# Optimization experiments

Measured on AMD Instinct MI355X. Metric: run time of the kernel, lower is better.

The kernel has to match this reference:

```python
import jax, jax.numpy as jnp
import numpy as np

EMBED_DIM = 1024
ATTEN_DIM = 64


def setup_inputs() -> dict:
    key = jax.random.key(0)
    k_x, k_q, k_k, k_v = jax.random.split(key, 4)
    B, S = 4, 4096
    scale = 1.0 / np.sqrt(EMBED_DIM)
    x = jax.random.normal(k_x, (B, S, EMBED_DIM), dtype=jnp.float32)
    # torch nn.Linear weights are [out_features, in_features]
    Wq = jax.random.normal(k_q, (ATTEN_DIM, EMBED_DIM), dtype=jnp.float32) * scale
    Wk = jax.random.normal(k_k, (ATTEN_DIM, EMBED_DIM), dtype=jnp.float32) * scale
    Wv = jax.random.normal(k_v, (ATTEN_DIM, EMBED_DIM), dtype=jnp.float32) * scale
    return {"x": x, "Wq": Wq, "Wk": Wk, "Wv": Wv}


def reference(x, Wq, Wk, Wv):
    # q, k, v: [B, S, D]
    q = jnp.einsum('bse,de->bsd', x, Wq)
    k = jnp.einsum('bse,de->bsd', x, Wk)
    v = jnp.einsum('bse,de->bsd', x, Wv)
    d = k.shape[-1]
    scores = jnp.einsum('bsd,btd->bst', q, k) / jnp.sqrt(jnp.float32(d))
    S = x.shape[1]
    causal = jnp.tril(jnp.ones((S, S), dtype=bool))
    scores = jnp.where(causal[None, :, :], scores, -jnp.inf)
    attn = jax.nn.softmax(scores, axis=-1)
    return jnp.einsum('bst,btd->bsd', attn, v)
```

## Files before the change

### kernel.cpp

```cpp
#include <hip/hip_runtime.h>
#include <hip/hip_bf16.h>
#include <stdint.h>

typedef __attribute__((ext_vector_type(8))) short  short8;
typedef __attribute__((ext_vector_type(4))) short  short4v;
typedef __attribute__((ext_vector_type(4))) float  float4v;

#define MFMA16(a, b, c) __builtin_amdgcn_mfma_f32_16x16x32_bf16((a), (b), (c), 0, 0, 0)

#define S_LEN  4096
#define NBATCH 4
#define EMB    1024
#define DD     64
#define NROWS  (NBATCH * S_LEN)
#define SCL2   0.1803368801111204f

static __device__ __forceinline__ short f2bf(float f) {
  uint32_t u = __float_as_uint(f);
  return (short)((u + 0x7FFFu + ((u >> 16) & 1u)) >> 16);
}
static __device__ __forceinline__ unsigned pk2(float a, float b) {
  union { __hip_bfloat162 h; unsigned u; } z;
  z.h = __float22bfloat162_rn(make_float2(a, b));
  return z.u;
}
static __device__ __forceinline__ short8 cvt8(float4v a, float4v b) {
  union { unsigned u[4]; short8 s; } z;
  z.u[0] = pk2(a[0], a[1]); z.u[1] = pk2(a[2], a[3]);
  z.u[2] = pk2(b[0], b[1]); z.u[3] = pk2(b[2], b[3]);
  return z.s;
}
static __device__ __forceinline__ short4v cvt4(float4v a) {
  union { unsigned u[2]; short4v s; } z;
  z.u[0] = pk2(a[0], a[1]); z.u[1] = pk2(a[2], a[3]);
  return z.s;
}

__global__ void wcvt_kernel(const float* __restrict__ Wq, const float* __restrict__ Wk,
                            const float* __restrict__ Wv, short* __restrict__ Wb2) {
  const int t   = blockIdx.x * 256 + threadIdx.x;
  const int row = t >> 7;
  const int k   = (t & 127) * 8;
  const float* src = (row < 64) ? (Wq + (size_t)row * EMB)
                   : (row < 128) ? (Wk + (size_t)(row - 64) * EMB)
                                 : (Wv + (size_t)(row - 128) * EMB);
  float4v a = *(const float4v*)(src + k);
  float4v b = *(const float4v*)(src + k + 4);
  *(short8*)(Wb2 + (((k >> 5) * 192 + row) << 5) + (k & 31)) = cvt8(a, b);
}

#define ASTR 40
#define BSTR 40

__global__ __launch_bounds__(256, 2) void qkv_kernel(
    const float* __restrict__ x, const short* __restrict__ Wb2,
    short* __restrict__ Qb, short* __restrict__ Kb, short* __restrict__ Vt) {
  __shared__ short As[2][32 * ASTR];
  __shared__ short Bs[2][192 * BSTR];

  const int tid  = threadIdx.x;
  const int w    = tid >> 6;
  const int lane = tid & 63;
  const int ln   = lane & 15;
  const int quad = lane >> 4;
  const int m0   = blockIdx.x * 32;
  const int rf   = w & 1;
  const int ch   = w >> 1;

  const int ar = tid >> 3, ac = (tid & 7) * 4;
  const float* xp = x + (size_t)(m0 + ar) * EMB + ac;

  const float4v zz = {0.f, 0.f, 0.f, 0.f};
  float4v acc[6];
#pragma unroll
  for (int f = 0; f < 6; ++f) acc[f] = zz;

  float4v apf = *(const float4v*)(xp);
  short8 bpf[3];
#pragma unroll
  for (int j = 0; j < 3; ++j)
    bpf[j] = *(const short8*)(Wb2 + (j * 256 + tid) * 8);

  int buf = 0;
  for (int s = 0; s < 32; ++s) {
    *(short4v*)&As[buf][ar * ASTR + ac] = cvt4(apf);
#pragma unroll
    for (int j = 0; j < 3; ++j) {
      const int i = j * 256 + tid;
      *(short8*)&Bs[buf][(i >> 2) * BSTR + (i & 3) * 8] = bpf[j];
    }
    __syncthreads();
    if (s + 1 < 32) {
      apf = *(const float4v*)(xp + (s + 1) * 32);
#pragma unroll
      for (int j = 0; j < 3; ++j)
        bpf[j] = *(const short8*)(Wb2 + (size_t)(s + 1) * 6144 + (j * 256 + tid) * 8);
    }
    const short8 af = *(const short8*)&As[buf][(rf * 16 + ln) * ASTR + quad * 8];
    if (ch == 0) {
#pragma unroll
      for (int f = 0; f < 6; ++f) {
        const short8 bf = *(const short8*)&Bs[buf][((f) * 16 + ln) * BSTR + quad * 8];
        acc[f] = MFMA16(af, bf, acc[f]);
      }
    } else {
#pragma unroll
      for (int f = 0; f < 2; ++f) {
        const short8 bf = *(const short8*)&Bs[buf][((6 + f) * 16 + ln) * BSTR + quad * 8];
        acc[f] = MFMA16(af, bf, acc[f]);
      }
#pragma unroll
      for (int f = 2; f < 6; ++f) {
        const short8 bf = *(const short8*)&Bs[buf][((6 + f) * 16 + ln) * BSTR + quad * 8];
        acc[f] = MFMA16(bf, af, acc[f]);
      }
    }
    buf ^= 1;
  }

  const int b  = m0 >> 12;
  const int sb = m0 & (S_LEN - 1);
  if (ch == 0) {
#pragma unroll
    for (int f = 0; f < 6; ++f)
#pragma unroll
      for (int r = 0; r < 4; ++r) {
        const int row = m0 + rf * 16 + quad * 4 + r;
        if (f < 4) Qb[(size_t)row * DD + f * 16 + ln] = f2bf(acc[f][r]);
        else       Kb[(size_t)row * DD + (f - 4) * 16 + ln] = f2bf(acc[f][r]);
      }
  } else {
#pragma unroll
    for (int f = 0; f < 2; ++f)
#pragma unroll
      for (int r = 0; r < 4; ++r) {
        const int row = m0 + rf * 16 + quad * 4 + r;
        Kb[(size_t)row * DD + 32 + f * 16 + ln] = f2bf(acc[f][r]);
      }
#pragma unroll
    for (int f = 2; f < 6; ++f)
#pragma unroll
      for (int r = 0; r < 4; ++r) {
        const int d = (f - 2) * 16 + quad * 4 + r;
        Vt[((size_t)b * DD + d) * S_LEN + sb + rf * 16 + ln] = f2bf(acc[f][r]);
      }
  }
}

#define PSTR 72

__global__ __launch_bounds__(256, 2) void attn_kernel(
    const short* __restrict__ Qb, const short* __restrict__ Kb,
    const short* __restrict__ Vt, float* __restrict__ out) {
  __shared__ float Olds[4][32][64];
  __shared__ float llds[4][32];
  __shared__ short pbuf[4][32 * PSTR];

  const int tid  = threadIdx.x;
  const int w    = tid >> 6;
  const int lane = tid & 63;
  const int ln   = lane & 15;
  const int quad = lane >> 4;
  const int g    = blockIdx.x;
  const int b    = (g & 7) >> 1;
  const int band = ((g >> 3) << 1) | (g & 1);
  const int qb   = band * 32;
  const int qg0  = b * S_LEN + qb;

  short8 aQ[2][2];
#pragma unroll
  for (int rfi = 0; rfi < 2; ++rfi)
#pragma unroll
    for (int h = 0; h < 2; ++h)
      aQ[rfi][h] = *(const short8*)(Qb + (size_t)(qg0 + rfi * 16 + ln) * DD + h * 32 + quad * 8);

  const short* Kbase = Kb + (size_t)b * S_LEN * DD;
  const short* Vbase = Vt + (size_t)b * DD * S_LEN;
  short* pb = &pbuf[w][0];

  const float4v zz = {0.f, 0.f, 0.f, 0.f};
  float4v o[2][4];
  float lp[2][4];
#pragma unroll
  for (int rfi = 0; rfi < 2; ++rfi)
#pragma unroll
    for (int d = 0; d < 4; ++d) { o[rfi][d] = zz; lp[rfi][d] = 0.f; }

  const int T = (qb + 95) >> 6;

  short8 Kc[4][2], Kn[4][2];
#pragma unroll
  for (int c = 0; c < 4; ++c)
#pragma unroll
    for (int h = 0; h < 2; ++h)
      Kc[c][h] = *(const short8*)(Kbase + (size_t)(w * 64 + c * 16 + ln) * DD + h * 32 + quad * 8);

  for (int it = w; it < T; it += 4) {
    const int kv0 = it * 64;
    short8 Vc[4][2];
#pragma unroll
    for (int d = 0; d < 4; ++d)
#pragma unroll
      for (int h = 0; h < 2; ++h)
        Vc[d][h] = *(const short8*)(Vbase + (size_t)(d * 16 + ln) * S_LEN + kv0 + h * 32 + quad * 8);

    float4v s[2][4];
#pragma unroll
    for (int rfi = 0; rfi < 2; ++rfi)
#pragma unroll
      for (int c = 0; c < 4; ++c) {
        s[rfi][c] = MFMA16(aQ[rfi][0], Kc[c][0], zz);
        s[rfi][c] = MFMA16(aQ[rfi][1], Kc[c][1], s[rfi][c]);
      }

    const int kvn = (it + 4 < T) ? (it + 4) * 64 : 0;
#pragma unroll
    for (int c = 0; c < 4; ++c)
#pragma unroll
      for (int h = 0; h < 2; ++h)
        Kn[c][h] = *(const short8*)(Kbase + (size_t)(kvn + c * 16 + ln) * DD + h * 32 + quad * 8);

    const bool needmask = (kv0 + 63) > qb;
#pragma unroll
    for (int rfi = 0; rfi < 2; ++rfi) {
      float p[4][4];
#pragma unroll
      for (int c = 0; c < 4; ++c)
#pragma unroll
        for (int r = 0; r < 4; ++r) {
          float e = exp2f(fminf(s[rfi][c][r] * SCL2, 43.0f));
          if (needmask && (kv0 + c * 16 + ln > qb + rfi * 16 + quad * 4 + r)) e = 0.f;
          p[c][r] = e;
        }
#pragma unroll
      for (int r = 0; r < 4; ++r)
        lp[rfi][r] += p[0][r] + p[1][r] + p[2][r] + p[3][r];
#pragma unroll
      for (int c = 0; c < 4; ++c)
#pragma unroll
        for (int r = 0; r < 4; ++r)
          pb[(rfi * 16 + quad * 4 + r) * PSTR + c * 16 + ln] = f2bf(p[c][r]);
    }
    asm volatile("s_waitcnt lgkmcnt(0)" ::: "memory");
    short8 aP[2][2];
#pragma unroll
    for (int rfi = 0; rfi < 2; ++rfi)
#pragma unroll
      for (int h = 0; h < 2; ++h)
        aP[rfi][h] = *(const short8*)&pb[(rfi * 16 + ln) * PSTR + h * 32 + quad * 8];
#pragma unroll
    for (int rfi = 0; rfi < 2; ++rfi)
#pragma unroll
      for (int d = 0; d < 4; ++d) {
        o[rfi][d] = MFMA16(aP[rfi][0], Vc[d][0], o[rfi][d]);
        o[rfi][d] = MFMA16(aP[rfi][1], Vc[d][1], o[rfi][d]);
      }
#pragma unroll
    for (int c = 0; c < 4; ++c)
#pragma unroll
      for (int h = 0; h < 2; ++h)
        Kc[c][h] = Kn[c][h];
  }

#pragma unroll
  for (int rfi = 0; rfi < 2; ++rfi)
#pragma unroll
    for (int r = 0; r < 4; ++r) {
      float lr = lp[rfi][r];
      lr += __shfl_xor(lr, 1);
      lr += __shfl_xor(lr, 2);
      lr += __shfl_xor(lr, 4);
      lr += __shfl_xor(lr, 8);
      if (ln == 0) llds[w][rfi * 16 + quad * 4 + r] = lr;
#pragma unroll
      for (int d = 0; d < 4; ++d)
        Olds[w][rfi * 16 + quad * 4 + r][d * 16 + ln] = o[rfi][d][r];
    }
  __syncthreads();

#pragma unroll
  for (int j = 0; j < 8; ++j) {
    const int idx = tid + j * 256;
    const int row = idx >> 6, col = idx & 63;
    const float sum = Olds[0][row][col] + Olds[1][row][col] +
                      Olds[2][row][col] + Olds[3][row][col];
    const float lt = llds[0][row] + llds[1][row] + llds[2][row] + llds[3][row];
    out[(size_t)(qg0 + row) * DD + col] = sum / lt;
  }
}

extern "C" void kernel_launch(void* const* d_in, const int* in_sizes, int n_in,
                              void* d_out, int out_size, void* d_ws, size_t ws_size,
                              hipStream_t stream) {
  const float* x  = (const float*)d_in[0];
  const float* Wq = (const float*)d_in[1];
  const float* Wk = (const float*)d_in[2];
  const float* Wv = (const float*)d_in[3];

  short* Qb  = (short*)d_ws;
  short* Kb  = Qb + (size_t)NROWS * DD;
  short* Vt  = Kb + (size_t)NROWS * DD;
  short* Wb2 = Vt + (size_t)NROWS * DD;

  wcvt_kernel<<<dim3(96), dim3(256), 0, stream>>>(Wq, Wk, Wv, Wb2);
  qkv_kernel<<<dim3(NROWS / 32), dim3(256), 0, stream>>>(x, Wb2, Qb, Kb, Vt);
  attn_kernel<<<dim3(NBATCH * 128), dim3(256), 0, stream>>>(Qb, Kb, Vt, (float*)d_out);
}
```

Baseline: 168.9 us.

## Drop LDS staging in QKV projection and reorder attention bands longest-first

The QKV projection kernel now has each block handle 16 rows. Each wave loads its x and weight fragments straight from global memory into registers, so the LDS staging and per-step barriers are gone, and occupancy is raised to 4 blocks per CU. The attention kernel dispatches query bands in reverse order so the longest causal bands start first, and it stores P as fp32 in a shared buffer that is reused for the output reduction. Together these target barrier overhead, LDS footprint and load imbalance. In exchange, the projection redundantly reloads weights per block with no shared-memory reuse, and the P traffic through LDS doubles.

```diff
diff --git a/kernel.cpp b/kernel.cpp
--- a/kernel.cpp
+++ b/kernel.cpp
@@ -28,11 +28,6 @@
   union { unsigned u[4]; short8 s; } z;
   z.u[0] = pk2(a[0], a[1]); z.u[1] = pk2(a[2], a[3]);
   z.u[2] = pk2(b[0], b[1]); z.u[3] = pk2(b[2], b[3]);
-  return z.s;
-}
-static __device__ __forceinline__ short4v cvt4(float4v a) {
-  union { unsigned u[2]; short4v s; } z;
-  z.u[0] = pk2(a[0], a[1]); z.u[1] = pk2(a[2], a[3]);
   return z.s;
 }
 
@@ -49,112 +44,66 @@
   *(short8*)(Wb2 + (((k >> 5) * 192 + row) << 5) + (k & 31)) = cvt8(a, b);
 }
 
-#define ASTR 40
-#define BSTR 40
-
-__global__ __launch_bounds__(256, 2) void qkv_kernel(
+__global__ __launch_bounds__(256, 4) void qkv_kernel(
     const float* __restrict__ x, const short* __restrict__ Wb2,
     short* __restrict__ Qb, short* __restrict__ Kb, short* __restrict__ Vt) {
-  __shared__ short As[2][32 * ASTR];
-  __shared__ short Bs[2][192 * BSTR];
-
   const int tid  = threadIdx.x;
   const int w    = tid >> 6;
   const int lane = tid & 63;
   const int ln   = lane & 15;
   const int quad = lane >> 4;
-  const int m0   = blockIdx.x * 32;
-  const int rf   = w & 1;
-  const int ch   = w >> 1;
-
-  const int ar = tid >> 3, ac = (tid & 7) * 4;
-  const float* xp = x + (size_t)(m0 + ar) * EMB + ac;
+  const int m0   = blockIdx.x * 16;
+
+  const float* xp = x + (size_t)(m0 + ln) * EMB + quad * 8;
+  const short* wp[3];
+#pragma unroll
+  for (int i = 0; i < 3; ++i)
+    wp[i] = Wb2 + (size_t)(i * 64 + w * 16 + ln) * 32 + quad * 8;
 
   const float4v zz = {0.f, 0.f, 0.f, 0.f};
-  float4v acc[6];
-#pragma unroll
-  for (int f = 0; f < 6; ++f) acc[f] = zz;
-
-  float4v apf = *(const float4v*)(xp);
+  float4v acc[3] = {zz, zz, zz};
+
+  float4v a0 = *(const float4v*)(xp);
+  float4v a1 = *(const float4v*)(xp + 4);
   short8 bpf[3];
 #pragma unroll
-  for (int j = 0; j < 3; ++j)
-    bpf[j] = *(const short8*)(Wb2 + (j * 256 + tid) * 8);
-
-  int buf = 0;
+  for (int i = 0; i < 3; ++i) bpf[i] = *(const short8*)(wp[i]);
+
   for (int s = 0; s < 32; ++s) {
-    *(short4v*)&As[buf][ar * ASTR + ac] = cvt4(apf);
-#pragma unroll
-    for (int j = 0; j < 3; ++j) {
-      const int i = j * 256 + tid;
-      *(short8*)&Bs[buf][(i >> 2) * BSTR + (i & 3) * 8] = bpf[j];
-    }
-    __syncthreads();
-    if (s + 1 < 32) {
-      apf = *(const float4v*)(xp + (s + 1) * 32);
-#pragma unroll
-      for (int j = 0; j < 3; ++j)
-        bpf[j] = *(const short8*)(Wb2 + (size_t)(s + 1) * 6144 + (j * 256 + tid) * 8);
-    }
-    const short8 af = *(const short8*)&As[buf][(rf * 16 + ln) * ASTR + quad * 8];
-    if (ch == 0) {
-#pragma unroll
-      for (int f = 0; f < 6; ++f) {
-        const short8 bf = *(const short8*)&Bs[buf][((f) * 16 + ln) * BSTR + quad * 8];
-        acc[f] = MFMA16(af, bf, acc[f]);
-      }
-    } else {
-#pragma unroll
-      for (int f = 0; f < 2; ++f) {
-        const short8 bf = *(const short8*)&Bs[buf][((6 + f) * 16 + ln) * BSTR + quad * 8];
-        acc[f] = MFMA16(af, bf, acc[f]);
-      }
-#pragma unroll
-      for (int f = 2; f < 6; ++f) {
-        const short8 bf = *(const short8*)&Bs[buf][((6 + f) * 16 + ln) * BSTR + quad * 8];
-        acc[f] = MFMA16(bf, af, acc[f]);
-      }
-    }
-    buf ^= 1;
+    const short8 xf = cvt8(a0, a1);
+    short8 bf[3];
+#pragma unroll
+    for (int i = 0; i < 3; ++i) bf[i] = bpf[i];
+    const int sn = (s + 1 < 32) ? s + 1 : 31;
+    a0 = *(const float4v*)(xp + sn * 32);
+    a1 = *(const float4v*)(xp + sn * 32 + 4);
+#pragma unroll
+    for (int i = 0; i < 3; ++i)
+      bpf[i] = *(const short8*)(wp[i] + (size_t)sn * 6144);
+    acc[0] = MFMA16(xf, bf[0], acc[0]);
+    acc[1] = MFMA16(xf, bf[1], acc[1]);
+    acc[2] = MFMA16(bf[2], xf, acc[2]);
   }
 
   const int b  = m0 >> 12;
   const int sb = m0 & (S_LEN - 1);
-  if (ch == 0) {
-#pragma unroll
-    for (int f = 0; f < 6; ++f)
-#pragma unroll
-      for (int r = 0; r < 4; ++r) {
-        const int row = m0 + rf * 16 + quad * 4 + r;
-        if (f < 4) Qb[(size_t)row * DD + f * 16 + ln] = f2bf(acc[f][r]);
-        else       Kb[(size_t)row * DD + (f - 4) * 16 + ln] = f2bf(acc[f][r]);
-      }
-  } else {
-#pragma unroll
-    for (int f = 0; f < 2; ++f)
-#pragma unroll
-      for (int r = 0; r < 4; ++r) {
-        const int row = m0 + rf * 16 + quad * 4 + r;
-        Kb[(size_t)row * DD + 32 + f * 16 + ln] = f2bf(acc[f][r]);
-      }
-#pragma unroll
-    for (int f = 2; f < 6; ++f)
-#pragma unroll
-      for (int r = 0; r < 4; ++r) {
-        const int d = (f - 2) * 16 + quad * 4 + r;
-        Vt[((size_t)b * DD + d) * S_LEN + sb + rf * 16 + ln] = f2bf(acc[f][r]);
-      }
-  }
-}
-
-#define PSTR 72
-
-__global__ __launch_bounds__(256, 2) void attn_kernel(
+#pragma unroll
+  for (int r = 0; r < 4; ++r) {
+    const int row = m0 + quad * 4 + r;
+    Qb[(size_t)row * DD + w * 16 + ln] = f2bf(acc[0][r]);
+    Kb[(size_t)row * DD + w * 16 + ln] = f2bf(acc[1][r]);
+    const int d = w * 16 + quad * 4 + r;
+    Vt[((size_t)b * DD + d) * S_LEN + sb + ln] = f2bf(acc[2][r]);
+  }
+}
+
+#define PSTRW 76
+
+__global__ __launch_bounds__(256, 4) void attn_kernel(
     const short* __restrict__ Qb, const short* __restrict__ Kb,
     const short* __restrict__ Vt, float* __restrict__ out) {
-  __shared__ float Olds[4][32][64];
+  __shared__ float sbuf[4][32 * PSTRW];
   __shared__ float llds[4][32];
-  __shared__ short pbuf[4][32 * PSTR];
 
   const int tid  = threadIdx.x;
   const int w    = tid >> 6;
@@ -162,8 +111,8 @@
   const int ln   = lane & 15;
   const int quad = lane >> 4;
   const int g    = blockIdx.x;
-  const int b    = (g & 7) >> 1;
-  const int band = ((g >> 3) << 1) | (g & 1);
+  const int b    = (g >> 1) & 3;
+  const int band = 127 - (((g >> 3) << 1) | (g & 1));
   const int qb   = band * 32;
   const int qg0  = b * S_LEN + qb;
 
@@ -176,7 +125,7 @@
 
   const short* Kbase = Kb + (size_t)b * S_LEN * DD;
   const short* Vbase = Vt + (size_t)b * DD * S_LEN;
-  short* pb = &pbuf[w][0];
+  float* pw = &sbuf[w][0];
 
   const float4v zz = {0.f, 0.f, 0.f, 0.f};
   float4v o[2][4];
@@ -239,15 +188,18 @@
       for (int c = 0; c < 4; ++c)
 #pragma unroll
         for (int r = 0; r < 4; ++r)
-          pb[(rfi * 16 + quad * 4 + r) * PSTR + c * 16 + ln] = f2bf(p[c][r]);
+          pw[(rfi * 16 + quad * 4 + r) * PSTRW + c * 16 + ln] = p[c][r];
     }
     asm volatile("s_waitcnt lgkmcnt(0)" ::: "memory");
     short8 aP[2][2];
 #pragma unroll
     for (int rfi = 0; rfi < 2; ++rfi)
 #pragma unroll
-      for (int h = 0; h < 2; ++h)
-        aP[rfi][h] = *(const short8*)&pb[(rfi * 16 + ln) * PSTR + h * 32 + quad * 8];
+      for (int h = 0; h < 2; ++h) {
+        const float4v lo = *(const float4v*)&pw[(rfi * 16 + ln) * PSTRW + h * 32 + quad * 8];
+        const float4v hi = *(const float4v*)&pw[(rfi * 16 + ln) * PSTRW + h * 32 + quad * 8 + 4];
+        aP[rfi][h] = cvt8(lo, hi);
+      }
 #pragma unroll
     for (int rfi = 0; rfi < 2; ++rfi)
 #pragma unroll
@@ -274,7 +226,7 @@
       if (ln == 0) llds[w][rfi * 16 + quad * 4 + r] = lr;
 #pragma unroll
       for (int d = 0; d < 4; ++d)
-        Olds[w][rfi * 16 + quad * 4 + r][d * 16 + ln] = o[rfi][d][r];
+        pw[(rfi * 16 + quad * 4 + r) * 64 + d * 16 + ln] = o[rfi][d][r];
     }
   __syncthreads();
 
@@ -282,8 +234,8 @@
   for (int j = 0; j < 8; ++j) {
     const int idx = tid + j * 256;
     const int row = idx >> 6, col = idx & 63;
-    const float sum = Olds[0][row][col] + Olds[1][row][col] +
-                      Olds[2][row][col] + Olds[3][row][col];
+    const float sum = sbuf[0][row * 64 + col] + sbuf[1][row * 64 + col] +
+                      sbuf[2][row * 64 + col] + sbuf[3][row * 64 + col];
     const float lt = llds[0][row] + llds[1][row] + llds[2][row] + llds[3][row];
     out[(size_t)(qg0 + row) * DD + col] = sum / lt;
   }
@@ -303,6 +255,6 @@
   short* Wb2 = Vt + (size_t)NROWS * DD;
 
   wcvt_kernel<<<dim3(96), dim3(256), 0, stream>>>(Wq, Wk, Wv, Wb2);
-  qkv_kernel<<<dim3(NROWS / 32), dim3(256), 0, stream>>>(x, Wb2, Qb, Kb, Vt);
+  qkv_kernel<<<dim3(NROWS / 16), dim3(256), 0, stream>>>(x, Wb2, Qb, Kb, Vt);
   attn_kernel<<<dim3(NBATCH * 128), dim3(256), 0, stream>>>(Qb, Kb, Vt, (float*)d_out);
 }
```

Result: slower. 254.6 us (+50.7%).
